# Kernel optimization log

Measured on AMD Instinct MI355X. Metric: run time of the kernel, lower is better.

Reference implementation:

```python
import jax, jax.numpy as jnp
import numpy as np

EPS = 1e-5            # BatchNorm3d eps (running_mean=0, running_var=1 at init)
SCALE = 0.025         # patchmatch_interval_scale
NEIGHBORS = 9         # evaluate_neighbors
PROP_OUT = 1          # propagation_out_range - 1


def conv1x1(x, w):
    # 1x1x1 Conv3d, no bias: x [B,C,D,H,W], w [O,C]
    return jnp.einsum('bcdhw,oc->bodhw', x, w)


def conv_bn_relu(x, w, g, b):
    # ConvBnReLU3D with BN at init stats (mean 0, var 1)
    y = conv1x1(x, w)
    y = g[None, :, None, None, None] * y / jnp.sqrt(1.0 + EPS) + b[None, :, None, None, None]
    return jax.nn.relu(y)


def neighbor_gather_sum(x, offset):
    # x [B,D,H,W]; offset [B,2*NEIGHBORS,H,W]
    # Reflection-pad then take 9 statically-offset windows at two dilations,
    # weight each by per-pixel offsets, and average the two scales.
    B, D, H, W = x.shape
    side = int(np.sqrt(NEIGHBORS))                 # 3
    p1 = side // 2 + PROP_OUT                      # 2
    p2 = p1 * 2                                    # 4
    X1 = jnp.pad(x, ((0, 0), (0, 0), (p1, p1), (p1, p1)), mode='reflect')
    X2 = jnp.pad(x, ((0, 0), (0, 0), (p2, p2), (p2, p2)), mode='reflect')
    acc = jnp.zeros_like(x)
    for s in range(NEIGHBORS):
        iy = (s // side) * (PROP_OUT + 1)
        ix = (s % side) * (PROP_OUT + 1)
        f1 = offset[:, s, None] * X2[:, :, 2 * iy:2 * iy + H, 2 * ix:2 * ix + W]
        f = offset[:, s + NEIGHBORS, None] * X1[:, :, iy:iy + H, ix:ix + W]
        acc = acc + (f + f1) * 0.5
    return acc


def setup_inputs():
    key = jax.random.key(0)
    ks = jax.random.split(key, 10)
    B, G, D, H, W = 2, 8, 16, 256, 320
    x1 = jax.random.normal(ks[0], (B, G, D, H, W), jnp.float32)
    offset = jax.random.uniform(ks[1], (B, 2 * NEIGHBORS, H, W), jnp.float32)
    depth_min = jnp.full((B,), 425.0, jnp.float32)
    depth_max = jnp.full((B,), 935.0, jnp.float32)
    depth_sample = 425.0 + 510.0 * jax.random.uniform(ks[2], (B, D, H, W), jnp.float32)
    w = lambda k, s: 0.1 * jax.random.normal(k, s, jnp.float32)
    return dict(
        x1=x1, offset=offset, depth_sample=depth_sample,
        depth_min=depth_min, depth_max=depth_max,
        s_w0=w(ks[3], (16, G)), s_g0=jnp.ones((16,)), s_b0=jnp.zeros((16,)),
        s_w1=w(ks[4], (8, 16)), s_g1=jnp.ones((8,)), s_b1=jnp.zeros((8,)),
        s_w2=w(ks[5], (1, 8)), s_bias2=jnp.zeros((1,)),
        p_w0=w(ks[6], (16, G)), p_g0=jnp.ones((16,)), p_b0=jnp.zeros((16,)),
        p_w1=w(ks[7], (8, 16)), p_g1=jnp.ones((8,)), p_b1=jnp.zeros((8,)),
        p_w2=w(ks[8], (1, 8)), p_bias2=jnp.zeros((1,)),
    )


def reference(x1, offset, depth_sample, depth_min, depth_max,
              s_w0, s_g0, s_b0, s_w1, s_g1, s_b1, s_w2, s_bias2,
              p_w0, p_g0, p_b0, p_w1, p_g1, p_b1, p_w2, p_bias2):
    # --- PixelwiseNet: per-pixel view weight from the group cost volume ---
    h = conv_bn_relu(x1, p_w0, p_g0, p_b0)
    h = conv_bn_relu(h, p_w1, p_g1, p_b1)
    h = conv1x1(h, p_w2) + p_bias2[None, :, None, None, None]
    vw = jax.nn.sigmoid(h[:, 0])                   # [B,D,H,W]
    view_weight = jnp.max(vw, axis=1, keepdims=True)  # [B,1,H,W]

    # --- Depth_weight: adaptive neighbor depth-similarity weight ---
    inv_min = 1.0 / depth_min
    inv_max = 1.0 / depth_max
    xn = (1.0 / depth_sample - inv_max[:, None, None, None]) / \
         (inv_min - inv_max)[:, None, None, None]  # normalized inverse depth
    xg = neighbor_gather_sum(xn, offset)
    dw = jax.nn.sigmoid((2.0 - jnp.clip(jnp.abs(xg - xn) / SCALE, 0.0, 4.0)) * 2.0)

    # --- SimilarityNet on view-weighted cost volume ---
    x1w = x1 * view_weight[:, None]                # [B,G,D,H,W]
    s = conv_bn_relu(x1w, s_w0, s_g0, s_b0)
    s = conv_bn_relu(s, s_w1, s_g1, s_b1)
    s = (conv1x1(s, s_w2) + s_bias2[None, :, None, None, None])[:, 0]  # [B,D,H,W]
    score = neighbor_gather_sum(s, offset) * dw

    attn = jax.nn.softmax(score, axis=1)
    depth = jnp.sum(depth_sample * attn, axis=1)   # [B,H,W]
    return depth
```

## Files before the change

### kernel.cpp

```cpp
#include <hip/hip_runtime.h>
#include <math.h>

constexpr int B = 2, G = 8, D = 16, H = 256, W = 320;
constexpr int HW = H * W;
constexpr float EPS = 1e-5f;
constexpr int WSTRIDE = 320;

__device__ __forceinline__ float sigmoidf_(float x) {
    return 1.0f / (1.0f + __expf(-x));
}

__device__ __forceinline__ int reflect_(int i, int n) {
    return i < 0 ? -i : (i >= n ? 2 * n - 2 - i : i);
}

__global__ __launch_bounds__(256) void k_prep(
    const float* __restrict__ sw0, const float* __restrict__ sg0, const float* __restrict__ sb0,
    const float* __restrict__ sw1, const float* __restrict__ sg1, const float* __restrict__ sb1,
    const float* __restrict__ sw2, const float* __restrict__ sbias2,
    const float* __restrict__ pw0, const float* __restrict__ pg0, const float* __restrict__ pb0,
    const float* __restrict__ pw1, const float* __restrict__ pg1, const float* __restrict__ pb1,
    const float* __restrict__ pw2, const float* __restrict__ pbias2,
    float* __restrict__ wbuf)
{
    const int t = threadIdx.x;
    const float rs = rsqrtf(1.0f + EPS);
    if (t < 128) {
        wbuf[t]                 = pw0[t] * pg0[t >> 3] * rs;
        wbuf[128 + t]           = pw1[t] * pg1[t >> 4] * rs;
        wbuf[WSTRIDE + t]       = sw0[t] * sg0[t >> 3] * rs;
        wbuf[WSTRIDE + 128 + t] = sw1[t] * sg1[t >> 4] * rs;
    } else {
        const int u = t - 128;
        if (u < 8) {
            wbuf[256 + u] = pw2[u];
            wbuf[WSTRIDE + 256 + u] = sw2[u];
        } else if (u < 24) {
            wbuf[264 + (u - 8)] = pb0[u - 8];
            wbuf[WSTRIDE + 264 + (u - 8)] = sb0[u - 8];
        } else if (u < 32) {
            wbuf[280 + (u - 24)] = pb1[u - 24];
            wbuf[WSTRIDE + 280 + (u - 24)] = sb1[u - 24];
        } else if (u == 32) {
            wbuf[288] = pbias2[0];
            wbuf[WSTRIDE + 288] = sbias2[0];
        }
    }
}

__device__ __forceinline__ float mlpg_(const float* __restrict__ Wb, const float x[8])
{
    float l1[16];
    #pragma unroll
    for (int o = 0; o < 16; ++o) {
        float a = Wb[264 + o];
        #pragma unroll
        for (int c = 0; c < 8; ++c) a = fmaf(Wb[o * 8 + c], x[c], a);
        l1[o] = fmaxf(a, 0.0f);
    }
    float l2[8];
    #pragma unroll
    for (int o = 0; o < 8; ++o) {
        float a = Wb[280 + o];
        #pragma unroll
        for (int c = 0; c < 16; ++c) a = fmaf(Wb[128 + o * 16 + c], l1[c], a);
        l2[o] = fmaxf(a, 0.0f);
    }
    float h = Wb[288];
    #pragma unroll
    for (int c = 0; c < 8; ++c) h = fmaf(Wb[256 + c], l2[c], h);
    return h;
}

__global__ __launch_bounds__(1024, 8) void k_fused(
    const float* __restrict__ x1,
    const float* __restrict__ depth_sample,
    const float* __restrict__ depth_min, const float* __restrict__ depth_max,
    const float* __restrict__ wP, const float* __restrict__ wS,
    float* __restrict__ s_out, float* __restrict__ xn_out)
{
    __shared__ float red[16][64];

    const int tid = threadIdx.x;
    const int pi = tid & 63;
    const int dt = tid >> 6;
    const int pid = blockIdx.x * 64 + pi;
    const int b = pid / HW;
    const int p = pid - b * HW;

    const float* xp = x1 + ((size_t)(b * G * D) + dt) * HW + p;
    float x[8];
    #pragma unroll
    for (int g = 0; g < 8; ++g) x[g] = xp[(size_t)g * D * HW];

    red[dt][pi] = mlpg_(wP, x);
    __syncthreads();

    float mx = red[0][pi];
    #pragma unroll
    for (int k = 1; k < 16; ++k) mx = fmaxf(mx, red[k][pi]);
    const float vw = sigmoidf_(mx);

    #pragma unroll
    for (int g = 0; g < 8; ++g) x[g] *= vw;
    const float hS = mlpg_(wS, x);

    const size_t oidx = (size_t)(b * D + dt) * HW + p;
    s_out[oidx] = hS;

    const float inv_min = 1.0f / depth_min[b];
    const float inv_max = 1.0f / depth_max[b];
    const float rinv = 1.0f / (inv_min - inv_max);
    const float ds = depth_sample[oidx];
    xn_out[oidx] = (1.0f / ds - inv_max) * rinv;
}

__global__ __launch_bounds__(1024, 8) void k_score_depth(
    const float* __restrict__ s_arr, const float* __restrict__ xn,
    const float* __restrict__ offset, const float* __restrict__ depth_sample,
    float* __restrict__ out)
{
    __shared__ float off_lds[18][64];
    __shared__ float redM[16][64];
    __shared__ float redS[16][64];
    __shared__ float redA[16][64];

    const int bid = blockIdx.x;
    const int wg = (bid & 7) * 320 + (bid >> 3);

    const int tid = threadIdx.x;
    const int pi = tid & 63;
    const int dt = tid >> 6;
    const int pg0_ = wg * 64;
    const int b = pg0_ / HW;
    const int pb0 = pg0_ - b * HW;
    const int p = pb0 + pi;
    const int h = p / W;
    const int w = p - h * W;

    const float* ob = offset + (size_t)b * 18 * HW + pb0;
    for (int idx = tid; idx < 18 * 64; idx += 1024) {
        const int s = idx >> 6, qq = idx & 63;
        off_lds[s][qq] = ob[(size_t)s * HW + qq];
    }
    __syncthreads();

    int a1s[9], a2s[9];
    {
        int ry1[3], ry2[3], cx1[3], cx2[3];
        #pragma unroll
        for (int i = 0; i < 3; ++i) {
            ry1[i] = reflect_(h + (i - 1) * 2, H) * W;
            ry2[i] = reflect_(h + (i - 1) * 4, H) * W;
            cx1[i] = reflect_(w + (i - 1) * 2, W);
            cx2[i] = reflect_(w + (i - 1) * 4, W);
        }
        #pragma unroll
        for (int s = 0; s < 9; ++s) {
            a1s[s] = ry1[s / 3] + cx1[s % 3];
            a2s[s] = ry2[s / 3] + cx2[s % 3];
        }
    }

    const size_t bbase = (size_t)b * D * HW;
    const float* sd = s_arr + bbase + (size_t)dt * HW;
    const float* xd = xn + bbase + (size_t)dt * HW;

    float accs = 0.0f, accx = 0.0f;
    #pragma unroll
    for (int s = 0; s < 9; ++s) {
        const float w1 = off_lds[s + 9][pi];
        const float w2 = off_lds[s][pi];
        accs += 0.5f * (w1 * sd[a1s[s]] + w2 * sd[a2s[s]]);
        accx += 0.5f * (w1 * xd[a1s[s]] + w2 * xd[a2s[s]]);
    }
    const float xc = xd[p];
    const float diff = fminf(fabsf(accx - xc) * 40.0f, 4.0f);
    const float dwv = sigmoidf_((2.0f - diff) * 2.0f);
    const float score = accs * dwv;
    const float dsv = depth_sample[bbase + (size_t)dt * HW + p];

    redM[dt][pi] = score;
    __syncthreads();
    float m = redM[0][pi];
    #pragma unroll
    for (int k = 1; k < 16; ++k) m = fmaxf(m, redM[k][pi]);

    const float e = __expf(score - m);
    redS[dt][pi] = e;
    redA[dt][pi] = dsv * e;
    __syncthreads();

    if (dt == 0) {
        float sum = 0.0f, acc = 0.0f;
        #pragma unroll
        for (int k = 0; k < 16; ++k) { sum += redS[k][pi]; acc += redA[k][pi]; }
        out[pg0_ + pi] = acc / sum;
    }
}

extern "C" void kernel_launch(void* const* d_in, const int* in_sizes, int n_in,
                              void* d_out, int out_size, void* d_ws, size_t ws_size,
                              hipStream_t stream)
{
    const float* x1           = (const float*)d_in[0];
    const float* offset       = (const float*)d_in[1];
    const float* depth_sample = (const float*)d_in[2];
    const float* depth_min    = (const float*)d_in[3];
    const float* depth_max    = (const float*)d_in[4];
    const float* s_w0 = (const float*)d_in[5];
    const float* s_g0 = (const float*)d_in[6];
    const float* s_b0 = (const float*)d_in[7];
    const float* s_w1 = (const float*)d_in[8];
    const float* s_g1 = (const float*)d_in[9];
    const float* s_b1 = (const float*)d_in[10];
    const float* s_w2 = (const float*)d_in[11];
    const float* s_bias2 = (const float*)d_in[12];
    const float* p_w0 = (const float*)d_in[13];
    const float* p_g0 = (const float*)d_in[14];
    const float* p_b0 = (const float*)d_in[15];
    const float* p_w1 = (const float*)d_in[16];
    const float* p_g1 = (const float*)d_in[17];
    const float* p_b1 = (const float*)d_in[18];
    const float* p_w2 = (const float*)d_in[19];
    const float* p_bias2 = (const float*)d_in[20];

    float* s_arr = (float*)d_ws;
    float* xn    = s_arr + (size_t)B * D * HW;
    float* wbuf  = xn + (size_t)B * D * HW;

    k_prep<<<1, 256, 0, stream>>>(
        s_w0, s_g0, s_b0, s_w1, s_g1, s_b1, s_w2, s_bias2,
        p_w0, p_g0, p_b0, p_w1, p_g1, p_b1, p_w2, p_bias2, wbuf);

    k_fused<<<(B * HW) / 64, 1024, 0, stream>>>(
        x1, depth_sample, depth_min, depth_max,
        wbuf, wbuf + WSTRIDE, s_arr, xn);

    k_score_depth<<<(B * HW) / 64, 1024, 0, stream>>>(
        s_arr, xn, offset, depth_sample, (float*)d_out);
}
```

Before: 82.96 us.

## Run both per-pixel MLPs on fp16 MFMA with shared first layer

Replaces the scalar fp32 1x1-conv MLPs in the fused kernel with fp16 32x32x16 MFMA ops. The view-weight and similarity first layers are stacked into one 32-row weight tile, so a single MFMA computes both. The similarity layer-1 output is cached and scaled by the view weight afterwards, which is valid because the sigmoid weight is positive and factors out of the convolution. This cuts the VALU FMA work and the repeated weight loads, at the cost of fp16 rounding, cross-lane shuffles, and a smaller 256-thread block with vectorized stores.

```diff
diff --git a/kernel.cpp b/kernel.cpp
--- a/kernel.cpp
+++ b/kernel.cpp
@@ -4,14 +4,24 @@
 constexpr int B = 2, G = 8, D = 16, H = 256, W = 320;
 constexpr int HW = H * W;
 constexpr float EPS = 1e-5f;
-constexpr int WSTRIDE = 320;
+
+typedef _Float16 half8  __attribute__((ext_vector_type(8)));
+typedef _Float16 h2v    __attribute__((ext_vector_type(2)));
+typedef float    f32x16 __attribute__((ext_vector_type(16)));
+
+union H8U { half8 h; unsigned u[4]; uint4 u4; };
+union H2U { h2v h; unsigned u; };
+
+constexpr int WB_TOTAL = 832;
 
 __device__ __forceinline__ float sigmoidf_(float x) {
     return 1.0f / (1.0f + __expf(-x));
 }
-
 __device__ __forceinline__ int reflect_(int i, int n) {
     return i < 0 ? -i : (i >= n ? 2 * n - 2 - i : i);
+}
+__device__ __forceinline__ unsigned pack2_(float a, float b) {
+    H2U p; p.h.x = (_Float16)a; p.h.y = (_Float16)b; return p.u;
 }
 
 __global__ __launch_bounds__(256) void k_prep(
@@ -25,94 +35,218 @@
 {
     const int t = threadIdx.x;
     const float rs = rsqrtf(1.0f + EPS);
-    if (t < 128) {
-        wbuf[t]                 = pw0[t] * pg0[t >> 3] * rs;
-        wbuf[128 + t]           = pw1[t] * pg1[t >> 4] * rs;
-        wbuf[WSTRIDE + t]       = sw0[t] * sg0[t >> 3] * rs;
-        wbuf[WSTRIDE + 128 + t] = sw1[t] * sg1[t >> 4] * rs;
+    unsigned* wu = (unsigned*)wbuf;
+
+    if (t < 64) {
+        unsigned dw[4] = {0u, 0u, 0u, 0u};
+        if (t < 32) {
+            const int row = t;
+            #pragma unroll
+            for (int j = 0; j < 4; ++j) {
+                float a0, a1;
+                if (row < 16) {
+                    const float s = pg0[row] * rs;
+                    a0 = pw0[row * 8 + 2 * j] * s; a1 = pw0[row * 8 + 2 * j + 1] * s;
+                } else {
+                    const float s = sg0[row - 16] * rs;
+                    a0 = sw0[(row - 16) * 8 + 2 * j] * s; a1 = sw0[(row - 16) * 8 + 2 * j + 1] * s;
+                }
+                dw[j] = pack2_(a0, a1);
+            }
+        }
+        #pragma unroll
+        for (int j = 0; j < 4; ++j) wu[t * 4 + j] = dw[j];
+    } else if (t < 128) {
+        const int l = t - 64, row = l & 31, kb = (l >> 5) * 8;
+        unsigned dw[4] = {0u, 0u, 0u, 0u};
+        if (row < 8) {
+            const float s = pg1[row] * rs;
+            #pragma unroll
+            for (int j = 0; j < 4; ++j)
+                dw[j] = pack2_(pw1[row * 16 + kb + 2 * j] * s, pw1[row * 16 + kb + 2 * j + 1] * s);
+        }
+        #pragma unroll
+        for (int j = 0; j < 4; ++j) wu[256 + l * 4 + j] = dw[j];
+    } else if (t < 192) {
+        const int l = t - 128, row = l & 31, kb = (l >> 5) * 8;
+        unsigned dw[4] = {0u, 0u, 0u, 0u};
+        if (row < 8) {
+            const float s = sg1[row] * rs;
+            #pragma unroll
+            for (int j = 0; j < 4; ++j)
+                dw[j] = pack2_(sw1[row * 16 + kb + 2 * j] * s, sw1[row * 16 + kb + 2 * j + 1] * s);
+        }
+        #pragma unroll
+        for (int j = 0; j < 4; ++j) wu[512 + l * 4 + j] = dw[j];
     } else {
-        const int u = t - 128;
-        if (u < 8) {
-            wbuf[256 + u] = pw2[u];
-            wbuf[WSTRIDE + 256 + u] = sw2[u];
-        } else if (u < 24) {
-            wbuf[264 + (u - 8)] = pb0[u - 8];
-            wbuf[WSTRIDE + 264 + (u - 8)] = sb0[u - 8];
-        } else if (u < 32) {
-            wbuf[280 + (u - 24)] = pb1[u - 24];
-            wbuf[WSTRIDE + 280 + (u - 24)] = sb1[u - 24];
-        } else if (u == 32) {
-            wbuf[288] = pbias2[0];
-            wbuf[WSTRIDE + 288] = sbias2[0];
-        }
-    }
-}
-
-__device__ __forceinline__ float mlpg_(const float* __restrict__ Wb, const float x[8])
-{
-    float l1[16];
-    #pragma unroll
-    for (int o = 0; o < 16; ++o) {
-        float a = Wb[264 + o];
-        #pragma unroll
-        for (int c = 0; c < 8; ++c) a = fmaf(Wb[o * 8 + c], x[c], a);
-        l1[o] = fmaxf(a, 0.0f);
-    }
-    float l2[8];
-    #pragma unroll
-    for (int o = 0; o < 8; ++o) {
-        float a = Wb[280 + o];
-        #pragma unroll
-        for (int c = 0; c < 16; ++c) a = fmaf(Wb[128 + o * 16 + c], l1[c], a);
-        l2[o] = fmaxf(a, 0.0f);
-    }
-    float h = Wb[288];
-    #pragma unroll
-    for (int c = 0; c < 8; ++c) h = fmaf(Wb[256 + c], l2[c], h);
-    return h;
-}
-
-__global__ __launch_bounds__(1024, 8) void k_fused(
+        const int u = t - 192;
+        if (u < 16)      wbuf[768 + u] = pb0[u];
+        else if (u < 24) wbuf[784 + (u - 16)] = pb1[u - 16];
+        else if (u < 32) wbuf[792 + (u - 24)] = pw2[u - 24];
+        else if (u == 32) wbuf[800] = pbias2[0];
+        else if (u == 33) wbuf[801] = sbias2[0];
+        else if (u < 42) { const int j = u - 34; wu[804 + j] = pack2_(sb0[2 * j], sb0[2 * j + 1]); }
+        else if (u < 50) wbuf[812 + (u - 42)] = sb1[u - 42];
+        else if (u < 58) wbuf[820 + (u - 50)] = sw2[u - 50];
+    }
+}
+
+__global__ __launch_bounds__(256, 4) void k_fused(
     const float* __restrict__ x1,
     const float* __restrict__ depth_sample,
     const float* __restrict__ depth_min, const float* __restrict__ depth_max,
-    const float* __restrict__ wP, const float* __restrict__ wS,
+    const float* __restrict__ wbuf,
     float* __restrict__ s_out, float* __restrict__ xn_out)
 {
-    __shared__ float red[16][64];
+    __shared__ float h3buf[16][64];
+    __shared__ float vwbuf[64];
+    __shared__ float sbuf[16][64];
 
     const int tid = threadIdx.x;
-    const int pi = tid & 63;
-    const int dt = tid >> 6;
-    const int pid = blockIdx.x * 64 + pi;
-    const int b = pid / HW;
-    const int p = pid - b * HW;
-
-    const float* xp = x1 + ((size_t)(b * G * D) + dt) * HW + p;
-    float x[8];
+    const int wave = tid >> 6, lane = tid & 63;
+    const bool hi = (lane & 32) != 0;
+    const int c31 = lane & 31;
+
+    const int pid0 = blockIdx.x * 64;
+    const int b = pid0 / HW;
+    const int p0 = pid0 - b * HW;
+
+    const unsigned* wu = (const unsigned*)wbuf;
+
+    H8U aL1, aL2P, aL2S;
+    aL1.u4  = ((const uint4*)(wu))[lane];
+    aL2P.u4 = ((const uint4*)(wu + 256))[lane];
+    aL2S.u4 = ((const uint4*)(wu + 512))[lane];
+
+    const float bias2P = wbuf[800], bias2S = wbuf[801];
+    const f32x16 z16 = {};
+    const size_t gstride = (size_t)D * HW;
+
+    unsigned sst[8][4];
+
     #pragma unroll
-    for (int g = 0; g < 8; ++g) x[g] = xp[(size_t)g * D * HW];
-
-    red[dt][pi] = mlpg_(wP, x);
-    __syncthreads();
-
-    float mx = red[0][pi];
+    for (int g8 = 0; g8 < 8; ++g8) {
+        const int dt = wave * 4 + (g8 >> 1);
+        const int px = (g8 & 1) * 32 + c31;
+
+        H8U bx; bx.u[0] = bx.u[1] = bx.u[2] = bx.u[3] = 0u;
+        if (!hi) {
+            const float* xp = x1 + ((size_t)b * G * D + dt) * HW + p0 + px;
+            float v[8];
+            #pragma unroll
+            for (int g = 0; g < 8; ++g) v[g] = xp[g * gstride];
+            #pragma unroll
+            for (int j = 0; j < 4; ++j) bx.u[j] = pack2_(v[2 * j], v[2 * j + 1]);
+        }
+
+        f32x16 acc = __builtin_amdgcn_mfma_f32_32x32x16_f16(aL1.h, bx.h, z16, 0, 0, 0);
+
+        unsigned l1dw[4];
+        #pragma unroll
+        for (int j = 0; j < 4; ++j) {
+            const int rb0 = (2 * j & 3) + 8 * (2 * j >> 2);
+            const int rb1 = ((2 * j + 1) & 3) + 8 * ((2 * j + 1) >> 2);
+            const float bb0 = hi ? wbuf[768 + rb0 + 4] : wbuf[768 + rb0];
+            const float bb1 = hi ? wbuf[768 + rb1 + 4] : wbuf[768 + rb1];
+            const float e0 = fmaxf(acc[2 * j] + bb0, 0.0f);
+            const float e1 = fmaxf(acc[2 * j + 1] + bb1, 0.0f);
+            l1dw[j] = pack2_(e0, e1);
+        }
+        #pragma unroll
+        for (int j = 0; j < 4; ++j) sst[g8][j] = pack2_(acc[8 + 2 * j], acc[9 + 2 * j]);
+
+        const unsigned x0 = (unsigned)__shfl_xor((int)l1dw[0], 32);
+        const unsigned x1_ = (unsigned)__shfl_xor((int)l1dw[1], 32);
+        const unsigned x2 = (unsigned)__shfl_xor((int)l1dw[2], 32);
+        const unsigned x3 = (unsigned)__shfl_xor((int)l1dw[3], 32);
+        H8U b2;
+        b2.u[0] = hi ? x2 : l1dw[0];
+        b2.u[1] = hi ? x3 : l1dw[1];
+        b2.u[2] = hi ? l1dw[2] : x0;
+        b2.u[3] = hi ? l1dw[3] : x1_;
+
+        f32x16 acc2 = __builtin_amdgcn_mfma_f32_32x32x16_f16(aL2P.h, b2.h, z16, 0, 0, 0);
+
+        float part = 0.0f;
+        #pragma unroll
+        for (int r = 0; r < 4; ++r) {
+            const float bb = hi ? wbuf[784 + r + 4] : wbuf[784 + r];
+            const float ww = hi ? wbuf[792 + r + 4] : wbuf[792 + r];
+            part = fmaf(fmaxf(acc2[r] + bb, 0.0f), ww, part);
+        }
+        part += __shfl_xor(part, 32);
+        if (!hi) h3buf[dt][px] = part + bias2P;
+    }
+    __syncthreads();
+
+    if (tid < 64) {
+        float m = h3buf[0][tid];
+        #pragma unroll
+        for (int k = 1; k < 16; ++k) m = fmaxf(m, h3buf[k][tid]);
+        vwbuf[tid] = sigmoidf_(m);
+    }
+    __syncthreads();
+
     #pragma unroll
-    for (int k = 1; k < 16; ++k) mx = fmaxf(mx, red[k][pi]);
-    const float vw = sigmoidf_(mx);
-
-    #pragma unroll
-    for (int g = 0; g < 8; ++g) x[g] *= vw;
-    const float hS = mlpg_(wS, x);
-
-    const size_t oidx = (size_t)(b * D + dt) * HW + p;
-    s_out[oidx] = hS;
-
-    const float inv_min = 1.0f / depth_min[b];
-    const float inv_max = 1.0f / depth_max[b];
-    const float rinv = 1.0f / (inv_min - inv_max);
-    const float ds = depth_sample[oidx];
-    xn_out[oidx] = (1.0f / ds - inv_max) * rinv;
+    for (int g8 = 0; g8 < 8; ++g8) {
+        const int dt = wave * 4 + (g8 >> 1);
+        const int px = (g8 & 1) * 32 + c31;
+        const float vw = vwbuf[px];
+        h2v vwh; vwh.x = (_Float16)vw; vwh.y = (_Float16)vw;
+
+        const unsigned t0 = sst[g8][0], t1 = sst[g8][1], t2 = sst[g8][2], t3 = sst[g8][3];
+        const unsigned y0 = (unsigned)__shfl_xor((int)t0, 32);
+        const unsigned y1 = (unsigned)__shfl_xor((int)t1, 32);
+        const unsigned y2 = (unsigned)__shfl_xor((int)t2, 32);
+        const unsigned y3 = (unsigned)__shfl_xor((int)t3, 32);
+        unsigned src[4];
+        src[0] = hi ? y2 : t0;
+        src[1] = hi ? y3 : t1;
+        src[2] = hi ? t2 : y0;
+        src[3] = hi ? t3 : y1;
+
+        H8U b2s;
+        #pragma unroll
+        for (int j = 0; j < 4; ++j) {
+            H2U pv; pv.u = src[j];
+            H2U bb; bb.u = hi ? wu[804 + j + 4] : wu[804 + j];
+            h2v val = pv.h * vwh + bb.h;
+            h2v zz = {};
+            val = __builtin_elementwise_max(val, zz);
+            H2U o2; o2.h = val; b2s.u[j] = o2.u;
+        }
+
+        f32x16 acc3 = __builtin_amdgcn_mfma_f32_32x32x16_f16(aL2S.h, b2s.h, z16, 0, 0, 0);
+
+        float part = 0.0f;
+        #pragma unroll
+        for (int r = 0; r < 4; ++r) {
+            const float bb = hi ? wbuf[812 + r + 4] : wbuf[812 + r];
+            const float ww = hi ? wbuf[820 + r + 4] : wbuf[820 + r];
+            part = fmaf(fmaxf(acc3[r] + bb, 0.0f), ww, part);
+        }
+        part += __shfl_xor(part, 32);
+        if (!hi) sbuf[dt][px] = part + bias2S;
+    }
+    __syncthreads();
+
+    {
+        const int dt = tid >> 4;
+        const int px0 = (tid & 15) * 4;
+        const size_t o = ((size_t)(b * D + dt)) * HW + p0 + px0;
+        const float4 sv = *(const float4*)&sbuf[dt][px0];
+        *(float4*)(s_out + o) = sv;
+        const float inv_min = 1.0f / depth_min[b];
+        const float inv_max = 1.0f / depth_max[b];
+        const float rinv = 1.0f / (inv_min - inv_max);
+        const float4 dsv = *(const float4*)(depth_sample + o);
+        float4 xv;
+        xv.x = (1.0f / dsv.x - inv_max) * rinv;
+        xv.y = (1.0f / dsv.y - inv_max) * rinv;
+        xv.z = (1.0f / dsv.z - inv_max) * rinv;
+        xv.w = (1.0f / dsv.w - inv_max) * rinv;
+        *(float4*)(xn_out + o) = xv;
+    }
 }
 
 __global__ __launch_bounds__(1024, 8) void k_score_depth(
@@ -233,9 +367,9 @@
         s_w0, s_g0, s_b0, s_w1, s_g1, s_b1, s_w2, s_bias2,
         p_w0, p_g0, p_b0, p_w1, p_g1, p_b1, p_w2, p_bias2, wbuf);
 
-    k_fused<<<(B * HW) / 64, 1024, 0, stream>>>(
+    k_fused<<<(B * HW) / 64, 256, 0, stream>>>(
         x1, depth_sample, depth_min, depth_max,
-        wbuf, wbuf + WSTRIDE, s_arr, xn);
+        wbuf, s_arr, xn);
 
     k_score_depth<<<(B * HW) / 64, 1024, 0, stream>>>(
         s_arr, xn, offset, depth_sample, (float*)d_out);
```

Result: faster. 79.89 us (-3.7%).
